# Kernel optimization log

Hardware: AMD Instinct MI355X
Metric: run time of the kernel (lower is better)

Reference implementation:

```python
import jax, jax.numpy as jnp
import numpy as np
import math

N_HEADS = 16
HEAD_DIM = 128
D_MODEL = 2048
THETA = 10000.0
SLIDING_WINDOW = 1024


def _rope_cos_sin(seq_len, dtype):
    inv_freq = 1.0 / (THETA ** (jnp.arange(0, HEAD_DIM, 2, dtype=jnp.float32) / HEAD_DIM))
    t = jnp.arange(seq_len, dtype=jnp.float32)
    freqs = jnp.outer(t, inv_freq)              # [S, D/2]
    emb = jnp.concatenate([freqs, freqs], -1)   # [S, D]
    return jnp.cos(emb).astype(dtype), jnp.sin(emb).astype(dtype)


def _rotate_half(x):
    x1, x2 = jnp.split(x, 2, axis=-1)
    return jnp.concatenate([-x2, x1], axis=-1)


def setup_inputs() -> dict:
    key = jax.random.key(0)
    ks = jax.random.split(key, 5)
    B, S = 2, 2048
    scale = 0.02
    return {
        "hidden_states": jax.random.normal(ks[0], (B, S, D_MODEL), jnp.float32),
        "Wq": jax.random.normal(ks[1], (D_MODEL, D_MODEL), jnp.float32) * scale,
        "Wk": jax.random.normal(ks[2], (D_MODEL, D_MODEL), jnp.float32) * scale,
        "Wv": jax.random.normal(ks[3], (D_MODEL, D_MODEL), jnp.float32) * scale,
        "Wo": jax.random.normal(ks[4], (D_MODEL, D_MODEL), jnp.float32) * scale,
    }


def reference(hidden_states, Wq, Wk, Wv, Wo):
    B, S, _ = hidden_states.shape
    dt = hidden_states.dtype

    def proj(x, W):  # torch Linear: x @ W^T -> [B, H, S, Dh]
        y = jnp.einsum('bsd,ed->bse', x, W)
        return y.reshape(B, S, N_HEADS, HEAD_DIM).transpose(0, 2, 1, 3)

    q = proj(hidden_states, Wq)
    k = proj(hidden_states, Wk)
    v = proj(hidden_states, Wv)

    cos, sin = _rope_cos_sin(S, dt)  # [S, Dh]
    cos = cos[None, None]
    sin = sin[None, None]
    q = q * cos + _rotate_half(q) * sin
    k = k * cos + _rotate_half(k) * sin

    scores = jnp.einsum('bhqd,bhkd->bhqk', q, k) / math.sqrt(HEAD_DIM)
    i = jnp.arange(S)[:, None]
    j = jnp.arange(S)[None, :]
    causal_mask = j > i                       # triu(diagonal=1)
    window_mask = (j - i) >= SLIDING_WINDOW   # triu(diagonal=sliding_window), as in source
    mask = causal_mask | window_mask
    scores = jnp.where(mask[None, None], -jnp.inf, scores)

    attn = jax.nn.softmax(scores.astype(jnp.float32), axis=-1).astype(dt)
    out = jnp.einsum('bhqk,bhkd->bhqd', attn, v)
    out = out.transpose(0, 2, 1, 3).reshape(B, S, D_MODEL)
    return jnp.einsum('bsd,ed->bse', out, Wo)
```

## Files before the change

kernel.cpp:

```cpp
#include <hip/hip_runtime.h>
#include <hip/hip_bf16.h>

typedef unsigned short u16;
typedef unsigned int u32;
typedef __attribute__((ext_vector_type(8))) short bf16x8;
typedef __attribute__((ext_vector_type(4))) float f32x4;

#define D_MODEL 2048
#define N_HEADS 16
#define HEAD_DIM 128
#define SEQ 2048
#define BATCH 2
#define M_ROWS (BATCH * SEQ)

__device__ __forceinline__ u16 f2bf(float f) {
  union { float f; u32 u; } x; x.f = f;
  u32 r = x.u + 0x7fffu + ((x.u >> 16) & 1u);
  return (u16)(r >> 16);
}
__device__ __forceinline__ float bf2f(u16 h) {
  union { u32 u; float f; } x; x.u = ((u32)h) << 16;
  return x.f;
}

__device__ __forceinline__ void async_copy16(void* lds, const void* gptr) {
  __builtin_amdgcn_global_load_lds(
      (const __attribute__((address_space(1))) void*)gptr,
      (__attribute__((address_space(3))) void*)lds, 16, 0, 0);
}

__global__ __launch_bounds__(256) void cast_bf16_kernel(const float* __restrict__ in,
                                                        u16* __restrict__ out, int n4) {
  int i = blockIdx.x * blockDim.x + threadIdx.x;
  if (i >= n4) return;
  float4 v = reinterpret_cast<const float4*>(in)[i];
  ushort4 o;
  o.x = f2bf(v.x); o.y = f2bf(v.y); o.z = f2bf(v.z); o.w = f2bf(v.w);
  reinterpret_cast<ushort4*>(out)[i] = o;
}

__global__ __launch_bounds__(256) void rope_table_kernel(float* __restrict__ cosT,
                                                         float* __restrict__ sinT) {
  int idx = blockIdx.x * blockDim.x + threadIdx.x;
  int s = idx >> 6, i = idx & 63;
  float invf = powf(10000.0f, -((float)(2 * i)) / 128.0f);
  float ang = (float)s * invf;
  cosT[idx] = cosf(ang);
  sinT[idx] = sinf(ang);
}

__global__ __launch_bounds__(256) void rope_apply_kernel(u16* __restrict__ Q, u16* __restrict__ K,
                                                         const float* __restrict__ cosT,
                                                         const float* __restrict__ sinT) {
  int idx = blockIdx.x * blockDim.x + threadIdx.x;
  u16* X = blockIdx.y ? K : Q;
  int i = idx & 63;
  int s = (idx >> 6) & (SEQ - 1);
  float c = cosT[(s << 6) + i], sn = sinT[(s << 6) + i];
  size_t base = ((size_t)(idx >> 17) * SEQ + s) * HEAD_DIM;
  float x1 = bf2f(X[base + i]);
  float x2 = bf2f(X[base + i + 64]);
  X[base + i] = f2bf(x1 * c - x2 * sn);
  X[base + i + 64] = f2bf(x2 * c + x1 * sn);
}

__global__ __launch_bounds__(256) void vtrans_kernel(const u16* __restrict__ V,
                                                     u16* __restrict__ Vt) {
  __shared__ u16 t[64][72];
  int bh = blockIdx.z, s0 = blockIdx.x * 64, d0 = blockIdx.y * 64;
  int tid = threadIdx.x;
#pragma unroll
  for (int p = 0; p < 2; ++p) {
    int r = p * 32 + (tid >> 3), c8 = tid & 7;
    *(uint4*)&t[r][c8 * 8] =
        *(const uint4*)&V[((size_t)bh * SEQ + s0 + r) * HEAD_DIM + d0 + c8 * 8];
  }
  __syncthreads();
#pragma unroll
  for (int p = 0; p < 2; ++p) {
    int d = p * 32 + (tid >> 3), s8 = tid & 7;
    u16 tmp[8];
#pragma unroll
    for (int j = 0; j < 8; ++j) tmp[j] = t[s8 * 8 + j][d];
    *(uint4*)&Vt[((size_t)bh * HEAD_DIM + d0 + d) * SEQ + s0 + s8 * 8] = *(uint4*)tmp;
  }
}

template <int MODE>
__global__ __launch_bounds__(256) void gemm_bt_kernel(
    const u16* __restrict__ A, const u16* __restrict__ B0, const u16* __restrict__ B1,
    const u16* __restrict__ B2, u16* __restrict__ Y0, u16* __restrict__ Y1,
    u16* __restrict__ Y2, float* __restrict__ OUT) {
  constexpr int KD = 2048;
  __shared__ u16 As[128 * 64];
  __shared__ u16 Bs[128 * 64];
  const int m0 = blockIdx.x * 128;
  const int n0 = blockIdx.y * 128;
  const u16* B = B0;
  u16* Y = Y0;
  if (MODE == 0) {
    if (blockIdx.z == 1) { B = B1; Y = Y1; }
    else if (blockIdx.z == 2) { B = B2; Y = Y2; }
  }
  const int tid = threadIdx.x;
  const int w = tid >> 6, l = tid & 63;
  const int wr = w >> 1, wc = w & 1;
  const int lrow = l & 15, lgrp = l >> 4;
  const int srow_in = l >> 3;
  const int sgcol = (((l & 7) ^ (l >> 3)) * 8);

  f32x4 acc[4][4];
#pragma unroll
  for (int mi = 0; mi < 4; ++mi)
#pragma unroll
    for (int ni = 0; ni < 4; ++ni) acc[mi][ni] = f32x4{0.f, 0.f, 0.f, 0.f};

  const u16* Ap = A + (size_t)m0 * KD;
  const u16* Bp = B + (size_t)n0 * KD;

  for (int k0 = 0; k0 < KD; k0 += 64) {
#pragma unroll
    for (int p = 0; p < 4; ++p) {
      int ig = w * 4 + p;
      int row = ig * 8 + srow_in;
      async_copy16(&As[ig * 512], &Ap[(size_t)row * KD + k0 + sgcol]);
      async_copy16(&Bs[ig * 512], &Bp[(size_t)row * KD + k0 + sgcol]);
    }
    __syncthreads();
#pragma unroll
    for (int ks = 0; ks < 2; ++ks) {
      bf16x8 af[4], bfr[4];
#pragma unroll
      for (int mi = 0; mi < 4; ++mi) {
        int row = wr * 64 + mi * 16 + lrow;
        int u = (ks * 4 + lgrp) ^ (row & 7);
        af[mi] = *(const bf16x8*)&As[row * 64 + u * 8];
      }
#pragma unroll
      for (int ni = 0; ni < 4; ++ni) {
        int row = wc * 64 + ni * 16 + lrow;
        int u = (ks * 4 + lgrp) ^ (row & 7);
        bfr[ni] = *(const bf16x8*)&Bs[row * 64 + u * 8];
      }
#pragma unroll
      for (int mi = 0; mi < 4; ++mi)
#pragma unroll
        for (int ni = 0; ni < 4; ++ni)
          acc[mi][ni] =
              __builtin_amdgcn_mfma_f32_16x16x32_bf16(af[mi], bfr[ni], acc[mi][ni], 0, 0, 0);
    }
    __syncthreads();
  }

#pragma unroll
  for (int mi = 0; mi < 4; ++mi)
#pragma unroll
    for (int ni = 0; ni < 4; ++ni)
#pragma unroll
      for (int r = 0; r < 4; ++r) {
        int m = m0 + wr * 64 + mi * 16 + lgrp * 4 + r;
        int n = n0 + wc * 64 + ni * 16 + lrow;
        if (MODE == 0) {
          int b = m >> 11, s = m & (SEQ - 1), h = n >> 7, d = n & 127;
          Y[(((size_t)b * N_HEADS + h) * SEQ + s) * HEAD_DIM + d] = f2bf(acc[mi][ni][r]);
        } else {
          OUT[(size_t)m * D_MODEL + n] = acc[mi][ni][r];
        }
      }
}

__global__ __launch_bounds__(256) void attn_kernel(const u16* __restrict__ Q,
                                                   const u16* __restrict__ Kg,
                                                   const u16* __restrict__ Vt,
                                                   u16* __restrict__ O) {
  __shared__ u16 Ks[64 * 128];
  __shared__ u16 Vs[128 * 64];
  __shared__ u16 Ps[4][16][72];
  const int bh = blockIdx.y;
  const int tid = threadIdx.x;
  const int w = tid >> 6, l = tid & 63;
  const int lrow = l & 15, lgrp = l >> 4;
  const float SCALE = 0.08838834764831845f;
  const float L2E = 1.4426950408889634f;
  const float NEG_INF = -__builtin_huge_valf();
  const int b = bh >> 4, h = bh & 15;

  const int krow = tid >> 4;
  const int kcg = tid & 15;
  const int vrow = tid >> 3;
  const int vcg = tid & 7;

  const u16* Kbase = Kg + (size_t)bh * SEQ * HEAD_DIM;
  const u16* Vbase = Vt + (size_t)bh * HEAD_DIM * SEQ;

  for (int pass = 0; pass < 2; ++pass) {
    const int qi = pass ? (31 - (int)blockIdx.x) : (int)blockIdx.x;
    const int q0 = qi * 64;
    const int ntiles = qi + 1;

    bf16x8 qf[4];
    {
      size_t qbase = ((size_t)bh * SEQ + q0 + w * 16 + lrow) * HEAD_DIM;
#pragma unroll
      for (int c = 0; c < 4; ++c) qf[c] = *(const bf16x8*)&Q[qbase + c * 32 + lgrp * 8];
    }
    f32x4 oacc[8];
#pragma unroll
    for (int dt = 0; dt < 8; ++dt) oacc[dt] = f32x4{0.f, 0.f, 0.f, 0.f};
    float mrun[4], lrun[4];
#pragma unroll
    for (int r = 0; r < 4; ++r) { mrun[r] = -1e30f; lrun[r] = 0.f; }

    uint4 kreg[4], vreg[4];
#pragma unroll
    for (int p = 0; p < 4; ++p)
      kreg[p] = *(const uint4*)&Kbase[(size_t)(p * 16 + krow) * HEAD_DIM + kcg * 8];
#pragma unroll
    for (int p = 0; p < 4; ++p)
      vreg[p] = *(const uint4*)&Vbase[(size_t)(p * 32 + vrow) * SEQ + vcg * 8];
#pragma unroll
    for (int p = 0; p < 4; ++p) {
      int r = p * 16 + krow;
      int pg = (kcg & 8) | ((kcg ^ r) & 7);
      *(uint4*)&Ks[r * 128 + pg * 8] = kreg[p];
    }
#pragma unroll
    for (int p = 0; p < 4; ++p) {
      int r = p * 32 + vrow;
      int pg = (vcg ^ r) & 7;
      *(uint4*)&Vs[r * 64 + pg * 8] = vreg[p];
    }
    __syncthreads();

    for (int t = 0; t < ntiles; ++t) {
      const int k0 = t * 64;
      const bool have_next = (t + 1) < ntiles;
      if (have_next) {
        const int kn = k0 + 64;
#pragma unroll
        for (int p = 0; p < 4; ++p)
          kreg[p] = *(const uint4*)&Kbase[(size_t)(kn + p * 16 + krow) * HEAD_DIM + kcg * 8];
#pragma unroll
        for (int p = 0; p < 4; ++p)
          vreg[p] = *(const uint4*)&Vbase[(size_t)(p * 32 + vrow) * SEQ + kn + vcg * 8];
      }

      f32x4 sc[4];
      __builtin_amdgcn_s_setprio(1);
#pragma unroll
      for (int kt = 0; kt < 4; ++kt) {
        f32x4 a = f32x4{0.f, 0.f, 0.f, 0.f};
#pragma unroll
        for (int c = 0; c < 4; ++c) {
          int r = kt * 16 + lrow;
          int g = c * 4 + lgrp;
          int pg = (g & 8) | ((g ^ r) & 7);
          bf16x8 kf = *(const bf16x8*)&Ks[r * 128 + pg * 8];
          a = __builtin_amdgcn_mfma_f32_16x16x32_bf16(qf[c], kf, a, 0, 0, 0);
        }
        sc[kt] = a;
      }
      __builtin_amdgcn_s_setprio(0);

      const bool bdry = (t == ntiles - 1);
#pragma unroll
      for (int kt = 0; kt < 4; ++kt)
#pragma unroll
        for (int r = 0; r < 4; ++r) {
          float s = sc[kt][r] * SCALE;
          if (bdry) {
            int j = k0 + kt * 16 + lrow;
            int i = q0 + w * 16 + lgrp * 4 + r;
            if (j > i) s = NEG_INF;
          }
          sc[kt][r] = s;
        }
      float resc[4], psum[4];
#pragma unroll
      for (int r = 0; r < 4; ++r) {
        float v = fmaxf(fmaxf(sc[0][r], sc[1][r]), fmaxf(sc[2][r], sc[3][r]));
        v = fmaxf(v, __shfl_xor(v, 1));
        v = fmaxf(v, __shfl_xor(v, 2));
        v = fmaxf(v, __shfl_xor(v, 4));
        v = fmaxf(v, __shfl_xor(v, 8));
        float mnew = fmaxf(mrun[r], v);
        resc[r] = exp2f((mrun[r] - mnew) * L2E);
        mrun[r] = mnew;
        psum[r] = 0.f;
      }
#pragma unroll
      for (int kt = 0; kt < 4; ++kt)
#pragma unroll
        for (int r = 0; r < 4; ++r) {
          float p = exp2f((sc[kt][r] - mrun[r]) * L2E);
          psum[r] += p;
          Ps[w][lgrp * 4 + r][kt * 16 + lrow] = f2bf(p);
        }
#pragma unroll
      for (int r = 0; r < 4; ++r) {
        float v = psum[r];
        v += __shfl_xor(v, 1);
        v += __shfl_xor(v, 2);
        v += __shfl_xor(v, 4);
        v += __shfl_xor(v, 8);
        lrun[r] = lrun[r] * resc[r] + v;
      }
#pragma unroll
      for (int dt = 0; dt < 8; ++dt)
#pragma unroll
        for (int r = 0; r < 4; ++r) oacc[dt][r] *= resc[r];
      bf16x8 pf[2];
#pragma unroll
      for (int kc = 0; kc < 2; ++kc)
        pf[kc] = *(const bf16x8*)&Ps[w][lrow][kc * 32 + lgrp * 8];
      __builtin_amdgcn_s_setprio(1);
#pragma unroll
      for (int dt = 0; dt < 8; ++dt) {
#pragma unroll
        for (int kc = 0; kc < 2; ++kc) {
          int r = dt * 16 + lrow;
          int g = kc * 4 + lgrp;
          int pg = (g ^ r) & 7;
          bf16x8 vf = *(const bf16x8*)&Vs[r * 64 + pg * 8];
          oacc[dt] = __builtin_amdgcn_mfma_f32_16x16x32_bf16(pf[kc], vf, oacc[dt], 0, 0, 0);
        }
      }
      __builtin_amdgcn_s_setprio(0);
      __syncthreads();
      if (have_next) {
#pragma unroll
        for (int p = 0; p < 4; ++p) {
          int r = p * 16 + krow;
          int pg = (kcg & 8) | ((kcg ^ r) & 7);
          *(uint4*)&Ks[r * 128 + pg * 8] = kreg[p];
        }
#pragma unroll
        for (int p = 0; p < 4; ++p) {
          int r = p * 32 + vrow;
          int pg = (vcg ^ r) & 7;
          *(uint4*)&Vs[r * 64 + pg * 8] = vreg[p];
        }
        __syncthreads();
      }
    }

    float inv[4];
#pragma unroll
    for (int r = 0; r < 4; ++r) inv[r] = 1.0f / lrun[r];
#pragma unroll
    for (int dt = 0; dt < 8; ++dt)
#pragma unroll
      for (int r = 0; r < 4; ++r) {
        int s = q0 + w * 16 + lgrp * 4 + r;
        size_t off = ((size_t)b * SEQ + s) * D_MODEL + h * HEAD_DIM + dt * 16 + lrow;
        O[off] = f2bf(oacc[dt][r] * inv[r]);
      }
  }
}

extern "C" void kernel_launch(void* const* d_in, const int* in_sizes, int n_in,
                              void* d_out, int out_size, void* d_ws, size_t ws_size,
                              hipStream_t stream) {
  const float* X = (const float*)d_in[0];
  const float* Wq = (const float*)d_in[1];
  const float* Wk = (const float*)d_in[2];
  const float* Wv = (const float*)d_in[3];
  const float* Wo = (const float*)d_in[4];
  float* OUT = (float*)d_out;
  char* ws = (char*)d_ws;

  u16* Xb = (u16*)(ws);
  u16* Wb0 = (u16*)(ws + (16u << 20));
  u16* Wb1 = Wb0 + 4194304;
  u16* Wb2 = Wb1 + 4194304;
  u16* Wb3 = Wb2 + 4194304;
  u16* Qb = (u16*)(ws + (48u << 20));
  u16* Kb = (u16*)(ws + (64u << 20));
  u16* Vb = (u16*)(ws + (80u << 20));
  u16* Vt = (u16*)(ws + (96u << 20));
  float* cosT = (float*)(ws + (112u << 20));
  float* sinT = cosT + SEQ * 64;
  u16* Ob = Xb;

  cast_bf16_kernel<<<8192, 256, 0, stream>>>(X, Xb, (M_ROWS * D_MODEL) / 4);
  cast_bf16_kernel<<<4096, 256, 0, stream>>>(Wq, Wb0, (D_MODEL * D_MODEL) / 4);
  cast_bf16_kernel<<<4096, 256, 0, stream>>>(Wk, Wb1, (D_MODEL * D_MODEL) / 4);
  cast_bf16_kernel<<<4096, 256, 0, stream>>>(Wv, Wb2, (D_MODEL * D_MODEL) / 4);
  cast_bf16_kernel<<<4096, 256, 0, stream>>>(Wo, Wb3, (D_MODEL * D_MODEL) / 4);
  rope_table_kernel<<<512, 256, 0, stream>>>(cosT, sinT);

  gemm_bt_kernel<0><<<dim3(32, 16, 3), 256, 0, stream>>>(Xb, Wb0, Wb1, Wb2, Qb, Kb, Vb, nullptr);
  rope_apply_kernel<<<dim3(16384, 2), 256, 0, stream>>>(Qb, Kb, cosT, sinT);
  vtrans_kernel<<<dim3(32, 2, 32), 256, 0, stream>>>(Vb, Vt);
  attn_kernel<<<dim3(16, 32), 256, 0, stream>>>(Qb, Kb, Vt, Ob);
  gemm_bt_kernel<1><<<dim3(32, 16, 1), 256, 0, stream>>>(Ob, Wb3, nullptr, nullptr, nullptr,
                                                         nullptr, nullptr, OUT);
}
```

Before: 517.2 us.

## Split attention KV range across two blocks and merge partial softmax results

Each attention query tile's key range is split into two halves processed by separate blocks, writing unnormalized partial outputs plus running max/sum, then a new merge kernel combines them and writes the final layout. This doubles the grid (512 to 1024 blocks) to improve occupancy/parallelism. The softmax scale and log2e factor are folded into Q during RoPE, and the P scratch buffer is aliased onto the K shared buffer to cut LDS usage, at the cost of an extra barrier per tile. The partial outputs are stored in bf16, which adds rounding error and an extra kernel launch plus memory traffic.

```diff
diff --git a/kernel.cpp b/kernel.cpp
--- a/kernel.cpp
+++ b/kernel.cpp
@@ -52,16 +52,18 @@
 __global__ __launch_bounds__(256) void rope_apply_kernel(u16* __restrict__ Q, u16* __restrict__ K,
                                                          const float* __restrict__ cosT,
                                                          const float* __restrict__ sinT) {
+  const float PSC = 0.08838834764831845f * 1.4426950408889634f;
   int idx = blockIdx.x * blockDim.x + threadIdx.x;
   u16* X = blockIdx.y ? K : Q;
+  float scl = blockIdx.y ? 1.0f : PSC;
   int i = idx & 63;
   int s = (idx >> 6) & (SEQ - 1);
   float c = cosT[(s << 6) + i], sn = sinT[(s << 6) + i];
   size_t base = ((size_t)(idx >> 17) * SEQ + s) * HEAD_DIM;
   float x1 = bf2f(X[base + i]);
   float x2 = bf2f(X[base + i + 64]);
-  X[base + i] = f2bf(x1 * c - x2 * sn);
-  X[base + i + 64] = f2bf(x2 * c + x1 * sn);
+  X[base + i] = f2bf((x1 * c - x2 * sn) * scl);
+  X[base + i + 64] = f2bf((x2 * c + x1 * sn) * scl);
 }
 
 __global__ __launch_bounds__(256) void vtrans_kernel(const u16* __restrict__ V,
@@ -169,34 +171,31 @@
       }
 }
 
-__global__ __launch_bounds__(256) void attn_kernel(const u16* __restrict__ Q,
-                                                   const u16* __restrict__ Kg,
-                                                   const u16* __restrict__ Vt,
-                                                   u16* __restrict__ O) {
+__global__ __launch_bounds__(256) void attn_split_kernel(
+    const u16* __restrict__ Q, const u16* __restrict__ Kg, const u16* __restrict__ Vt,
+    u16* __restrict__ OpH0, u16* __restrict__ OpH1, float2* __restrict__ Ml) {
   __shared__ u16 Ks[64 * 128];
   __shared__ u16 Vs[128 * 64];
-  __shared__ u16 Ps[4][16][72];
-  const int bh = blockIdx.y;
+  const int pr = blockIdx.x, hf = blockIdx.y, bh = blockIdx.z;
   const int tid = threadIdx.x;
   const int w = tid >> 6, l = tid & 63;
   const int lrow = l & 15, lgrp = l >> 4;
-  const float SCALE = 0.08838834764831845f;
-  const float L2E = 1.4426950408889634f;
   const float NEG_INF = -__builtin_huge_valf();
-  const int b = bh >> 4, h = bh & 15;
-
-  const int krow = tid >> 4;
-  const int kcg = tid & 15;
-  const int vrow = tid >> 3;
-  const int vcg = tid & 7;
+  u16* Ps_w = &Ks[w * 1152];
+
+  const int krow = tid >> 4, kcg = tid & 15;
+  const int vrow = tid >> 3, vcg = tid & 7;
 
   const u16* Kbase = Kg + (size_t)bh * SEQ * HEAD_DIM;
   const u16* Vbase = Vt + (size_t)bh * HEAD_DIM * SEQ;
 
   for (int pass = 0; pass < 2; ++pass) {
-    const int qi = pass ? (31 - (int)blockIdx.x) : (int)blockIdx.x;
+    const int qi = pass ? (31 - pr) : pr;
     const int q0 = qi * 64;
-    const int ntiles = qi + 1;
+    const int nt = qi + 1;
+    const int n0 = (nt + 1) >> 1;
+    const int tb = hf ? n0 : 0;
+    const int te = hf ? nt : n0;
 
     bf16x8 qf[4];
     {
@@ -212,29 +211,32 @@
     for (int r = 0; r < 4; ++r) { mrun[r] = -1e30f; lrun[r] = 0.f; }
 
     uint4 kreg[4], vreg[4];
-#pragma unroll
-    for (int p = 0; p < 4; ++p)
-      kreg[p] = *(const uint4*)&Kbase[(size_t)(p * 16 + krow) * HEAD_DIM + kcg * 8];
-#pragma unroll
-    for (int p = 0; p < 4; ++p)
-      vreg[p] = *(const uint4*)&Vbase[(size_t)(p * 32 + vrow) * SEQ + vcg * 8];
-#pragma unroll
-    for (int p = 0; p < 4; ++p) {
-      int r = p * 16 + krow;
-      int pg = (kcg & 8) | ((kcg ^ r) & 7);
-      *(uint4*)&Ks[r * 128 + pg * 8] = kreg[p];
-    }
-#pragma unroll
-    for (int p = 0; p < 4; ++p) {
-      int r = p * 32 + vrow;
-      int pg = (vcg ^ r) & 7;
-      *(uint4*)&Vs[r * 64 + pg * 8] = vreg[p];
-    }
-    __syncthreads();
-
-    for (int t = 0; t < ntiles; ++t) {
+    if (tb < te) {
+      const int kb = tb * 64;
+#pragma unroll
+      for (int p = 0; p < 4; ++p)
+        kreg[p] = *(const uint4*)&Kbase[(size_t)(kb + p * 16 + krow) * HEAD_DIM + kcg * 8];
+#pragma unroll
+      for (int p = 0; p < 4; ++p)
+        vreg[p] = *(const uint4*)&Vbase[(size_t)(p * 32 + vrow) * SEQ + kb + vcg * 8];
+#pragma unroll
+      for (int p = 0; p < 4; ++p) {
+        int r = p * 16 + krow;
+        int pg = (kcg & 8) | ((kcg ^ r) & 7);
+        *(uint4*)&Ks[r * 128 + pg * 8] = kreg[p];
+      }
+#pragma unroll
+      for (int p = 0; p < 4; ++p) {
+        int r = p * 32 + vrow;
+        int pg = (vcg ^ r) & 7;
+        *(uint4*)&Vs[r * 64 + pg * 8] = vreg[p];
+      }
+      __syncthreads();
+    }
+
+    for (int t = tb; t < te; ++t) {
       const int k0 = t * 64;
-      const bool have_next = (t + 1) < ntiles;
+      const bool have_next = (t + 1) < te;
       if (have_next) {
         const int kn = k0 + 64;
 #pragma unroll
@@ -261,13 +263,14 @@
         sc[kt] = a;
       }
       __builtin_amdgcn_s_setprio(0);
-
-      const bool bdry = (t == ntiles - 1);
+      __syncthreads();
+
+      const bool bdry = (t == nt - 1);
 #pragma unroll
       for (int kt = 0; kt < 4; ++kt)
 #pragma unroll
         for (int r = 0; r < 4; ++r) {
-          float s = sc[kt][r] * SCALE;
+          float s = sc[kt][r];
           if (bdry) {
             int j = k0 + kt * 16 + lrow;
             int i = q0 + w * 16 + lgrp * 4 + r;
@@ -284,7 +287,7 @@
         v = fmaxf(v, __shfl_xor(v, 4));
         v = fmaxf(v, __shfl_xor(v, 8));
         float mnew = fmaxf(mrun[r], v);
-        resc[r] = exp2f((mrun[r] - mnew) * L2E);
+        resc[r] = exp2f(mrun[r] - mnew);
         mrun[r] = mnew;
         psum[r] = 0.f;
       }
@@ -292,9 +295,9 @@
       for (int kt = 0; kt < 4; ++kt)
 #pragma unroll
         for (int r = 0; r < 4; ++r) {
-          float p = exp2f((sc[kt][r] - mrun[r]) * L2E);
+          float p = exp2f(sc[kt][r] - mrun[r]);
           psum[r] += p;
-          Ps[w][lgrp * 4 + r][kt * 16 + lrow] = f2bf(p);
+          Ps_w[(lgrp * 4 + r) * 72 + kt * 16 + lrow] = f2bf(p);
         }
 #pragma unroll
       for (int r = 0; r < 4; ++r) {
@@ -312,7 +315,7 @@
       bf16x8 pf[2];
 #pragma unroll
       for (int kc = 0; kc < 2; ++kc)
-        pf[kc] = *(const bf16x8*)&Ps[w][lrow][kc * 32 + lgrp * 8];
+        pf[kc] = *(const bf16x8*)&Ps_w[lrow * 72 + kc * 32 + lgrp * 8];
       __builtin_amdgcn_s_setprio(1);
 #pragma unroll
       for (int dt = 0; dt < 8; ++dt) {
@@ -344,18 +347,47 @@
       }
     }
 
-    float inv[4];
-#pragma unroll
-    for (int r = 0; r < 4; ++r) inv[r] = 1.0f / lrun[r];
+    u16* Op = hf ? OpH1 : OpH0;
 #pragma unroll
     for (int dt = 0; dt < 8; ++dt)
 #pragma unroll
       for (int r = 0; r < 4; ++r) {
         int s = q0 + w * 16 + lgrp * 4 + r;
-        size_t off = ((size_t)b * SEQ + s) * D_MODEL + h * HEAD_DIM + dt * 16 + lrow;
-        O[off] = f2bf(oacc[dt][r] * inv[r]);
-      }
+        Op[((size_t)bh * SEQ + s) * HEAD_DIM + dt * 16 + lrow] = f2bf(oacc[dt][r]);
+      }
+    if (lrow == 0) {
+#pragma unroll
+      for (int r = 0; r < 4; ++r) {
+        int s = q0 + w * 16 + lgrp * 4 + r;
+        Ml[hf * (32 * SEQ) + bh * SEQ + s] = float2{mrun[r], lrun[r]};
+      }
+    }
   }
+}
+
+__global__ __launch_bounds__(256) void attn_merge_kernel(const u16* __restrict__ O0,
+                                                         const u16* __restrict__ O1,
+                                                         const float2* __restrict__ Ml,
+                                                         u16* __restrict__ O) {
+  const int tid = threadIdx.x;
+  const int row = blockIdx.x * 16 + (tid >> 4);
+  const int d = (tid & 15) * 8;
+  float2 a = Ml[row];
+  float2 c = Ml[32 * SEQ + row];
+  float mx = fmaxf(a.x, c.x);
+  float w0 = exp2f(a.x - mx), w1 = exp2f(c.x - mx);
+  float inv = 1.0f / (w0 * a.y + w1 * c.y);
+  w0 *= inv; w1 *= inv;
+  size_t src = (size_t)row * HEAD_DIM + d;
+  bf16x8 v0 = *(const bf16x8*)&O0[src];
+  bf16x8 v1 = *(const bf16x8*)&O1[src];
+  u16 outv[8];
+#pragma unroll
+  for (int j = 0; j < 8; ++j)
+    outv[j] = f2bf(w0 * bf2f((u16)v0[j]) + w1 * bf2f((u16)v1[j]));
+  int bh = row >> 11, s = row & (SEQ - 1);
+  size_t dst = ((size_t)(bh >> 4) * SEQ + s) * D_MODEL + (bh & 15) * HEAD_DIM + d;
+  *(uint4*)&O[dst] = *(uint4*)outv;
 }
 
 extern "C" void kernel_launch(void* const* d_in, const int* in_sizes, int n_in,
@@ -381,6 +413,9 @@
   float* cosT = (float*)(ws + (112u << 20));
   float* sinT = cosT + SEQ * 64;
   u16* Ob = Xb;
+  u16* OpH0 = Vb;
+  u16* OpH1 = Wb0;
+  float2* Ml = (float2*)Wb2;
 
   cast_bf16_kernel<<<8192, 256, 0, stream>>>(X, Xb, (M_ROWS * D_MODEL) / 4);
   cast_bf16_kernel<<<4096, 256, 0, stream>>>(Wq, Wb0, (D_MODEL * D_MODEL) / 4);
@@ -392,7 +427,8 @@
   gemm_bt_kernel<0><<<dim3(32, 16, 3), 256, 0, stream>>>(Xb, Wb0, Wb1, Wb2, Qb, Kb, Vb, nullptr);
   rope_apply_kernel<<<dim3(16384, 2), 256, 0, stream>>>(Qb, Kb, cosT, sinT);
   vtrans_kernel<<<dim3(32, 2, 32), 256, 0, stream>>>(Vb, Vt);
-  attn_kernel<<<dim3(16, 32), 256, 0, stream>>>(Qb, Kb, Vt, Ob);
+  attn_split_kernel<<<dim3(16, 2, 32), 256, 0, stream>>>(Qb, Kb, Vt, OpH0, OpH1, Ml);
+  attn_merge_kernel<<<4096, 256, 0, stream>>>(OpH0, OpH1, Ml, Ob);
   gemm_bt_kernel<1><<<dim3(32, 16, 1), 256, 0, stream>>>(Ob, Wb3, nullptr, nullptr, nullptr,
                                                          nullptr, nullptr, OUT);
 }
```

Result: slower. 551.5 us (+6.6%).
